# Kernel tuning notes

Measured on AMD Instinct MI355X. Metric: run time of the kernel, lower is better.

Reference implementation:

```python
import jax, jax.numpy as jnp
import numpy as np

C_OP, C_M, C_A, C_OUT = 256, 256, 256, 256
P = T = M = 65536

def _mlp(x, w1, b1, w2, b2):
    h = jax.nn.leaky_relu(x @ w1 + b1)  # LeakyReLU default slope 0.01
    return h @ w2 + b2

def setup_inputs() -> dict:
    key = jax.random.key(0)
    ks = jax.random.split(key, 24)
    s = 0.02
    inp = {
        'operation_emb': jax.random.normal(ks[0], (50000, C_OP), jnp.float32),
        'machine_emb': jax.random.normal(ks[1], (10000, C_M), jnp.float32),
        'agv_emb': jax.random.normal(ks[2], (5000, C_A), jnp.float32),
        'wait_emb': jnp.zeros((C_OUT,), jnp.float32),
        'pick_w1': jax.random.normal(ks[3], (C_A + 2 * C_OP + C_M, 2 * C_OUT), jnp.float32) * s,
        'pick_b1': jnp.zeros((2 * C_OUT,), jnp.float32),
        'pick_w2': jax.random.normal(ks[4], (2 * C_OUT, C_OUT), jnp.float32) * s,
        'pick_b2': jnp.zeros((C_OUT,), jnp.float32),
        'trans_w1': jax.random.normal(ks[5], (C_A + C_M, 2 * C_OUT), jnp.float32) * s,
        'trans_b1': jnp.zeros((2 * C_OUT,), jnp.float32),
        'trans_w2': jax.random.normal(ks[6], (2 * C_OUT, C_OUT), jnp.float32) * s,
        'trans_b2': jnp.zeros((C_OUT,), jnp.float32),
        'move_w1': jax.random.normal(ks[7], (C_A + C_M, 2 * C_OUT), jnp.float32) * s,
        'move_b1': jnp.zeros((2 * C_OUT,), jnp.float32),
        'move_w2': jax.random.normal(ks[8], (2 * C_OUT, C_OUT), jnp.float32) * s,
        'move_b2': jnp.zeros((C_OUT,), jnp.float32),
        'pick_agv': jax.random.randint(ks[9], (P,), 0, 5000),
        'pick_op_from': jax.random.randint(ks[10], (P,), 0, 50000),
        'pick_op_to': jax.random.randint(ks[11], (P,), 0, 50000),
        'pick_machine': jax.random.randint(ks[12], (P,), 0, 10000),
        'trans_agv': jax.random.randint(ks[13], (T,), 0, 5000),
        'trans_machine': jax.random.randint(ks[14], (T,), 0, 10000),
        'move_agv': jax.random.randint(ks[15], (M,), 0, 5000),
        'move_machine': jax.random.randint(ks[16], (M,), 0, 10000),
        'n_wait': 1024,
    }
    return inp

def reference(operation_emb, machine_emb, agv_emb, wait_emb,
              pick_w1, pick_b1, pick_w2, pick_b2,
              trans_w1, trans_b1, trans_w2, trans_b2,
              move_w1, move_b1, move_w2, move_b2,
              pick_agv, pick_op_from, pick_op_to, pick_machine,
              trans_agv, trans_machine, move_agv, move_machine, n_wait):
    # wait actions: the shared learned wait embedding, tiled
    wait_out = jnp.broadcast_to(wait_emb, (n_wait, wait_emb.shape[0]))
    # pick: [AGV, op_from, op_to, machine] gather + concat + 2-layer MLP
    pick_in = jnp.concatenate([agv_emb[pick_agv], operation_emb[pick_op_from],
                               operation_emb[pick_op_to], machine_emb[pick_machine]], axis=-1)
    pick_out = _mlp(pick_in, pick_w1, pick_b1, pick_w2, pick_b2)
    # transport / move: [AGV, machine]
    trans_in = jnp.concatenate([agv_emb[trans_agv], machine_emb[trans_machine]], axis=-1)
    trans_out = _mlp(trans_in, trans_w1, trans_b1, trans_w2, trans_b2)
    move_in = jnp.concatenate([agv_emb[move_agv], machine_emb[move_machine]], axis=-1)
    move_out = _mlp(move_in, move_w1, move_b1, move_w2, move_b2)
    # stacked per-action encodings (actions grouped by type)
    return jnp.concatenate([wait_out, pick_out, trans_out, move_out], axis=0)
```

## Files before the change

### kernel.cpp

```cpp
#include <hip/hip_runtime.h>
#include <stdint.h>

typedef __bf16 b16x8 __attribute__((ext_vector_type(8)));
typedef float  f32x4 __attribute__((ext_vector_type(4)));
typedef unsigned short u16;
typedef unsigned int   u32;

#define W1T_P 0
#define W1T_T 524288
#define W1T_M 786432
#define W2T_P 1048576
#define W2T_T 1179648
#define W2T_M 1310720

#define STG_STRIDE 264
#define H_STRIDE   520
#define SMEM_U16   (64 * H_STRIDE)

__device__ __forceinline__ u16 f2bf(float x) {
    union { float f; u32 u; } v; v.f = x;
    u32 u = v.u;
    u += 0x7fffu + ((u >> 16) & 1u);
    return (u16)(u >> 16);
}
__device__ __forceinline__ f32x4 mfma16(b16x8 a, b16x8 b, f32x4 c) {
    return __builtin_amdgcn_mfma_f32_16x16x32_bf16(a, b, c, 0, 0, 0);
}
__device__ __forceinline__ b16x8 ld8(const u16* p) { return *(const b16x8*)p; }

__device__ __forceinline__ const float* tblFor(int type, int s,
        const float* agvT, const float* opT, const float* machT) {
    if (s == 0) return agvT;
    if (type != 0) return machT;
    return (s == 3) ? machT : opT;
}

__global__ void transpose_all(const float* __restrict__ pw1, const float* __restrict__ tw1,
                              const float* __restrict__ mw1, const float* __restrict__ pw2,
                              const float* __restrict__ tw2, const float* __restrict__ mw2,
                              u16* __restrict__ wsE)
{
    const int mat = blockIdx.y;
    const float* src; u16* dst; int R, C;
    switch (mat) {
        case 0: src = pw1; R = 1024; C = 512; dst = wsE + W1T_P; break;
        case 1: src = tw1; R = 512;  C = 512; dst = wsE + W1T_T; break;
        case 2: src = mw1; R = 512;  C = 512; dst = wsE + W1T_M; break;
        case 3: src = pw2; R = 512;  C = 256; dst = wsE + W2T_P; break;
        case 4: src = tw2; R = 512;  C = 256; dst = wsE + W2T_T; break;
        default: src = mw2; R = 512; C = 256; dst = wsE + W2T_M; break;
    }
    const int tilesC = C >> 5, tilesR = R >> 5;
    const int bx = blockIdx.x % tilesC, by = blockIdx.x / tilesC;
    if (by >= tilesR) return;
    __shared__ u16 tile[32][33];
    const int tx = threadIdx.x & 31, ty = threadIdx.x >> 5;
    #pragma unroll
    for (int i = 0; i < 4; ++i)
        tile[ty + i * 8][tx] = f2bf(src[(by * 32 + ty + i * 8) * C + bx * 32 + tx]);
    __syncthreads();
    #pragma unroll
    for (int i = 0; i < 4; ++i)
        dst[(bx * 32 + ty + i * 8) * R + by * 32 + tx] = tile[tx][ty + i * 8];
}

__global__ void wait_fill(const float* __restrict__ wait_emb, float* __restrict__ out, int n)
{
    int i = blockIdx.x * 256 + threadIdx.x;
    if (i < n) out[i] = wait_emb[i & 255];
}

__global__ __launch_bounds__(512, 4)
void mlp_kernel(const u16* __restrict__ wsE,
                const float* __restrict__ opTab, const float* __restrict__ machTab,
                const float* __restrict__ agvTab,
                const float* __restrict__ p_b1, const float* __restrict__ p_b2,
                const float* __restrict__ t_b1, const float* __restrict__ t_b2,
                const float* __restrict__ m_b1, const float* __restrict__ m_b2,
                const int* __restrict__ p_agv, const int* __restrict__ p_from,
                const int* __restrict__ p_to,  const int* __restrict__ p_mach,
                const int* __restrict__ t_agv, const int* __restrict__ t_mach,
                const int* __restrict__ m_agv, const int* __restrict__ m_mach,
                float* __restrict__ out,
                int n_wait, int rowsPerType, int nOp, int nMach, int nAgv)
{
    __shared__ __align__(16) u16 sMem[SMEM_U16];
    __shared__ int sIdx[256];
    u16* const sStg = sMem;
    u16* const sH   = sMem;

    const int type = blockIdx.y;
    const int row0 = blockIdx.x * 64;
    const int tid  = threadIdx.x;
    const int lane = tid & 63;
    const int wv   = tid >> 6;
    const int l15  = lane & 15;
    const int q    = lane >> 4;
    const int srow = tid >> 3;
    const int sc8  = tid & 7;

    int nseg;
    const u16 *w1t, *w2t;
    const float *b1, *b2;
    const int *i0, *i1, *i2, *i3;
    int outRowBase;
    if (type == 0) {
        nseg = 4;  w1t = wsE + W1T_P; w2t = wsE + W2T_P;
        b1 = p_b1; b2 = p_b2;
        i0 = p_agv; i1 = p_from; i2 = p_to; i3 = p_mach;
        outRowBase = n_wait;
    } else if (type == 1) {
        nseg = 2;  w1t = wsE + W1T_T; w2t = wsE + W2T_T;
        b1 = t_b1; b2 = t_b2;
        i0 = t_agv; i1 = t_mach; i2 = t_agv; i3 = t_mach;
        outRowBase = n_wait + rowsPerType;
    } else {
        nseg = 2;  w1t = wsE + W1T_M; w2t = wsE + W2T_M;
        b1 = m_b1; b2 = m_b2;
        i0 = m_agv; i1 = m_mach; i2 = m_agv; i3 = m_mach;
        outRowBase = n_wait + 2 * rowsPerType;
    }
    const int K1 = nseg << 8;

    if (tid < (nseg << 6)) {
        int seg = tid >> 6, r = tid & 63;
        const int* ip = (seg == 0) ? i0 : (seg == 1) ? i1 : (seg == 2) ? i2 : i3;
        int lim = (seg == 0) ? nAgv
                 : (type == 0) ? ((seg == 3) ? nMach : nOp) : nMach;
        int rr = row0 + r;
        if (rr >= rowsPerType) rr = rowsPerType - 1;
        int v = ip[rr];
        if (v < 0) v = 0;
        if (v >= lim) v = lim - 1;
        sIdx[tid] = v;
    }
    __syncthreads();

    int aAddr[4];
    #pragma unroll
    for (int t = 0; t < 4; ++t)
        aAddr[t] = (t * 16 + l15) * STG_STRIDE + q * 8;
    int wOff[4];
    #pragma unroll
    for (int u = 0; u < 4; ++u)
        wOff[u] = (wv * 64 + u * 16 + l15) * K1 + q * 8;

    f32x4 acc1[4][4];
    #pragma unroll
    for (int t = 0; t < 4; ++t)
        #pragma unroll
        for (int u = 0; u < 4; ++u)
            acc1[t][u] = (f32x4)0.f;

    for (int sg = 0; sg < nseg; ++sg) {
        if (sg) __syncthreads();
        {
            const float* src = tblFor(type, sg, agvTab, opTab, machTab)
                             + sIdx[(sg << 6) + srow] * 256 + sc8 * 32;
            f32x4 g[8];
            #pragma unroll
            for (int j = 0; j < 8; ++j)
                g[j] = *(const f32x4*)(src + j * 4);
            u16* dst = sStg + srow * STG_STRIDE + sc8 * 32;
            #pragma unroll
            for (int j = 0; j < 4; ++j) {
                b16x8 a;
                a[0] = (__bf16)g[2*j][0]; a[1] = (__bf16)g[2*j][1];
                a[2] = (__bf16)g[2*j][2]; a[3] = (__bf16)g[2*j][3];
                a[4] = (__bf16)g[2*j+1][0]; a[5] = (__bf16)g[2*j+1][1];
                a[6] = (__bf16)g[2*j+1][2]; a[7] = (__bf16)g[2*j+1][3];
                *(b16x8*)(dst + j * 8) = a;
            }
        }
        __syncthreads();

        const u16* wb = w1t + sg * 256;
        #pragma unroll
        for (int s8 = 0; s8 < 8; ++s8) {
            b16x8 aF[4], bF[4];
            #pragma unroll
            for (int t = 0; t < 4; ++t)
                aF[t] = *(const b16x8*)&sStg[aAddr[t] + s8 * 32];
            #pragma unroll
            for (int u = 0; u < 4; ++u)
                bF[u] = ld8(wb + wOff[u] + s8 * 32);
            #pragma unroll
            for (int t = 0; t < 4; ++t)
                #pragma unroll
                for (int u = 0; u < 4; ++u)
                    acc1[t][u] = mfma16(aF[t], bF[u], acc1[t][u]);
        }
    }
    __syncthreads();

    #pragma unroll
    for (int u = 0; u < 4; ++u) {
        int c = wv * 64 + u * 16 + l15;
        float bb = b1[c];
        #pragma unroll
        for (int t = 0; t < 4; ++t) {
            #pragma unroll
            for (int r = 0; r < 4; ++r) {
                float x = acc1[t][u][r] + bb;
                x = x > 0.f ? x : 0.01f * x;
                int row = t * 16 + q * 4 + r;
                sH[row * H_STRIDE + c] = f2bf(x);
            }
        }
    }
    __syncthreads();

    int w2Off[2];
    #pragma unroll
    for (int u = 0; u < 2; ++u)
        w2Off[u] = (wv * 32 + u * 16 + l15) * 512 + q * 8;

    f32x4 acc2[4][2];
    #pragma unroll
    for (int t = 0; t < 4; ++t)
        #pragma unroll
        for (int u = 0; u < 2; ++u)
            acc2[t][u] = (f32x4)0.f;

    #pragma unroll
    for (int s2 = 0; s2 < 16; ++s2) {
        b16x8 hF[4], bF[2];
        #pragma unroll
        for (int t = 0; t < 4; ++t)
            hF[t] = *(const b16x8*)&sH[(t * 16 + l15) * H_STRIDE + s2 * 32 + q * 8];
        #pragma unroll
        for (int u = 0; u < 2; ++u)
            bF[u] = ld8(w2t + w2Off[u] + s2 * 32);
        #pragma unroll
        for (int t = 0; t < 4; ++t)
            #pragma unroll
            for (int u = 0; u < 2; ++u)
                acc2[t][u] = mfma16(hF[t], bF[u], acc2[t][u]);
    }

    const int obase = (outRowBase + row0) * 256;
    #pragma unroll
    for (int u = 0; u < 2; ++u) {
        int c = wv * 32 + u * 16 + l15;
        float bb = b2[c];
        #pragma unroll
        for (int t = 0; t < 4; ++t) {
            #pragma unroll
            for (int r = 0; r < 4; ++r) {
                int row = t * 16 + q * 4 + r;
                if (row0 + row < rowsPerType)
                    __builtin_nontemporal_store(acc2[t][u][r] + bb,
                                                &out[obase + row * 256 + c]);
            }
        }
    }
}

extern "C" void kernel_launch(void* const* d_in, const int* in_sizes, int n_in,
                              void* d_out, int out_size, void* d_ws, size_t ws_size,
                              hipStream_t stream)
{
    const float* op_emb   = (const float*)d_in[0];
    const float* mach_emb = (const float*)d_in[1];
    const float* agv_emb  = (const float*)d_in[2];
    const float* wait_emb = (const float*)d_in[3];
    const float* pick_w1  = (const float*)d_in[4];
    const float* pick_b1  = (const float*)d_in[5];
    const float* pick_w2  = (const float*)d_in[6];
    const float* pick_b2  = (const float*)d_in[7];
    const float* trans_w1 = (const float*)d_in[8];
    const float* trans_b1 = (const float*)d_in[9];
    const float* trans_w2 = (const float*)d_in[10];
    const float* trans_b2 = (const float*)d_in[11];
    const float* move_w1  = (const float*)d_in[12];
    const float* move_b1  = (const float*)d_in[13];
    const float* move_w2  = (const float*)d_in[14];
    const float* move_b2  = (const float*)d_in[15];
    const int* pick_agv   = (const int*)d_in[16];
    const int* pick_from  = (const int*)d_in[17];
    const int* pick_to    = (const int*)d_in[18];
    const int* pick_mach  = (const int*)d_in[19];
    const int* trans_agv  = (const int*)d_in[20];
    const int* trans_mach = (const int*)d_in[21];
    const int* move_agv   = (const int*)d_in[22];
    const int* move_mach  = (const int*)d_in[23];

    const int P = in_sizes[16];
    const int T = in_sizes[20];
    const int M = in_sizes[22];
    const int n_wait = out_size / 256 - P - T - M;
    const int nOp   = in_sizes[0] / 256;
    const int nMach = in_sizes[1] / 256;
    const int nAgv  = in_sizes[2] / 256;

    u16* wsE = (u16*)d_ws;
    float* out = (float*)d_out;

    transpose_all<<<dim3(512, 6), 256, 0, stream>>>(pick_w1, trans_w1, move_w1,
                                                    pick_w2, trans_w2, move_w2, wsE);
    if (n_wait > 0)
        wait_fill<<<(n_wait * 256 + 255) / 256, 256, 0, stream>>>(
            wait_emb, out, n_wait * 256);

    mlp_kernel<<<dim3((P + 63) / 64, 3), 512, 0, stream>>>(
        wsE,
        op_emb, mach_emb, agv_emb,
        pick_b1, pick_b2, trans_b1, trans_b2, move_b1, move_b2,
        pick_agv, pick_from, pick_to, pick_mach,
        trans_agv, trans_mach, move_agv, move_mach,
        out, n_wait, P, nOp, nMach, nAgv);
}
```

Before: 666.2 us.

## Double-buffer gathered embedding segments and pre-convert embedding tables to bf16

Pre-converts the three embedding tables to bf16 in workspace when it is large enough, halving the bytes read per gathered row. Restructures the layer-1 loop to double-buffer the staging LDS: the next segment's gather is issued before the MFMAs on the current one and stored halfway through, which drops one barrier per segment. It also interleaves the three action types across a 1-D grid. The trade-offs are extra conversion kernels that read the full tables each call, and more LDS and registers per block.

```diff
diff --git a/kernel.cpp b/kernel.cpp
--- a/kernel.cpp
+++ b/kernel.cpp
@@ -12,10 +12,12 @@
 #define W2T_P 1048576
 #define W2T_T 1179648
 #define W2T_M 1310720
+#define WS_WEIGHTS_U16 1441792
 
 #define STG_STRIDE 264
+#define STG_BUF    (64 * STG_STRIDE)
 #define H_STRIDE   520
-#define SMEM_U16   (64 * H_STRIDE)
+#define SMEM_U16   (2 * STG_BUF)
 
 __device__ __forceinline__ u16 f2bf(float x) {
     union { float f; u32 u; } v; v.f = x;
@@ -30,6 +32,12 @@
 
 __device__ __forceinline__ const float* tblFor(int type, int s,
         const float* agvT, const float* opT, const float* machT) {
+    if (s == 0) return agvT;
+    if (type != 0) return machT;
+    return (s == 3) ? machT : opT;
+}
+__device__ __forceinline__ const u16* tb16For(int type, int s,
+        const u16* agvT, const u16* opT, const u16* machT) {
     if (s == 0) return agvT;
     if (type != 0) return machT;
     return (s == 3) ? machT : opT;
@@ -64,6 +72,19 @@
         dst[(bx * 32 + ty + i * 8) * R + by * 32 + tx] = tile[tx][ty + i * 8];
 }
 
+__global__ void cvt_f32_bf16(const float* __restrict__ src, u16* __restrict__ dst, int n)
+{
+    int i = (blockIdx.x * 256 + threadIdx.x) * 8;
+    if (i + 8 <= n) {
+        f32x4 a = *(const f32x4*)(src + i);
+        f32x4 b = *(const f32x4*)(src + i + 4);
+        b16x8 v;
+        v[0] = (__bf16)a[0]; v[1] = (__bf16)a[1]; v[2] = (__bf16)a[2]; v[3] = (__bf16)a[3];
+        v[4] = (__bf16)b[0]; v[5] = (__bf16)b[1]; v[6] = (__bf16)b[2]; v[7] = (__bf16)b[3];
+        *(b16x8*)(dst + i) = v;
+    }
+}
+
 __global__ void wait_fill(const float* __restrict__ wait_emb, float* __restrict__ out, int n)
 {
     int i = blockIdx.x * 256 + threadIdx.x;
@@ -74,6 +95,8 @@
 void mlp_kernel(const u16* __restrict__ wsE,
                 const float* __restrict__ opTab, const float* __restrict__ machTab,
                 const float* __restrict__ agvTab,
+                const u16* __restrict__ opT16, const u16* __restrict__ machT16,
+                const u16* __restrict__ agvT16, int useBf16,
                 const float* __restrict__ p_b1, const float* __restrict__ p_b2,
                 const float* __restrict__ t_b1, const float* __restrict__ t_b2,
                 const float* __restrict__ m_b1, const float* __restrict__ m_b2,
@@ -86,11 +109,11 @@
 {
     __shared__ __align__(16) u16 sMem[SMEM_U16];
     __shared__ int sIdx[256];
-    u16* const sStg = sMem;
-    u16* const sH   = sMem;
-
-    const int type = blockIdx.y;
-    const int row0 = blockIdx.x * 64;
+    u16* const sH = sMem;
+
+    const int bid  = blockIdx.x;
+    const int type = bid % 3;
+    const int row0 = (bid / 3) * 64;
     const int tid  = threadIdx.x;
     const int lane = tid & 63;
     const int wv   = tid >> 6;
@@ -152,35 +175,56 @@
         for (int u = 0; u < 4; ++u)
             acc1[t][u] = (f32x4)0.f;
 
+    if (useBf16) {
+        const u16* src = tb16For(type, 0, agvT16, opT16, machT16)
+                       + (size_t)sIdx[srow] * 256 + sc8 * 32;
+        b16x8 g0 = ld8(src), g1 = ld8(src + 8), g2 = ld8(src + 16), g3 = ld8(src + 24);
+        u16* dst = sMem + srow * STG_STRIDE + sc8 * 32;
+        *(b16x8*)(dst)      = g0; *(b16x8*)(dst + 8)  = g1;
+        *(b16x8*)(dst + 16) = g2; *(b16x8*)(dst + 24) = g3;
+    } else {
+        const float* src = tblFor(type, 0, agvTab, opTab, machTab)
+                         + (size_t)sIdx[srow] * 256 + sc8 * 32;
+        u16* dst = sMem + srow * STG_STRIDE + sc8 * 32;
+        #pragma unroll
+        for (int j = 0; j < 4; ++j) {
+            f32x4 a = *(const f32x4*)(src + j * 8);
+            f32x4 b = *(const f32x4*)(src + j * 8 + 4);
+            b16x8 v;
+            v[0]=(__bf16)a[0]; v[1]=(__bf16)a[1]; v[2]=(__bf16)a[2]; v[3]=(__bf16)a[3];
+            v[4]=(__bf16)b[0]; v[5]=(__bf16)b[1]; v[6]=(__bf16)b[2]; v[7]=(__bf16)b[3];
+            *(b16x8*)(dst + j * 8) = v;
+        }
+    }
+    __syncthreads();
+
+    int cur = 0;
     for (int sg = 0; sg < nseg; ++sg) {
-        if (sg) __syncthreads();
-        {
-            const float* src = tblFor(type, sg, agvTab, opTab, machTab)
-                             + sIdx[(sg << 6) + srow] * 256 + sc8 * 32;
-            f32x4 g[8];
-            #pragma unroll
-            for (int j = 0; j < 8; ++j)
-                g[j] = *(const f32x4*)(src + j * 4);
-            u16* dst = sStg + srow * STG_STRIDE + sc8 * 32;
-            #pragma unroll
-            for (int j = 0; j < 4; ++j) {
-                b16x8 a;
-                a[0] = (__bf16)g[2*j][0]; a[1] = (__bf16)g[2*j][1];
-                a[2] = (__bf16)g[2*j][2]; a[3] = (__bf16)g[2*j][3];
-                a[4] = (__bf16)g[2*j+1][0]; a[5] = (__bf16)g[2*j+1][1];
-                a[6] = (__bf16)g[2*j+1][2]; a[7] = (__bf16)g[2*j+1][3];
-                *(b16x8*)(dst + j * 8) = a;
+        const u16* sA = sMem + cur * STG_BUF;
+        const u16* wb = w1t + sg * 256;
+        const bool hasNext = (sg + 1) < nseg;
+
+        b16x8 g0, g1, g2, g3;
+        f32x4 pf[8];
+        if (hasNext) {
+            if (useBf16) {
+                const u16* src = tb16For(type, sg + 1, agvT16, opT16, machT16)
+                               + (size_t)sIdx[((sg + 1) << 6) + srow] * 256 + sc8 * 32;
+                g0 = ld8(src); g1 = ld8(src + 8); g2 = ld8(src + 16); g3 = ld8(src + 24);
+            } else {
+                const float* src = tblFor(type, sg + 1, agvTab, opTab, machTab)
+                                 + (size_t)sIdx[((sg + 1) << 6) + srow] * 256 + sc8 * 32;
+                #pragma unroll
+                for (int j = 0; j < 8; ++j) pf[j] = *(const f32x4*)(src + j * 4);
             }
         }
-        __syncthreads();
-
-        const u16* wb = w1t + sg * 256;
-        #pragma unroll
-        for (int s8 = 0; s8 < 8; ++s8) {
+
+        #pragma unroll
+        for (int s8 = 0; s8 < 4; ++s8) {
             b16x8 aF[4], bF[4];
             #pragma unroll
             for (int t = 0; t < 4; ++t)
-                aF[t] = *(const b16x8*)&sStg[aAddr[t] + s8 * 32];
+                aF[t] = *(const b16x8*)&sA[aAddr[t] + s8 * 32];
             #pragma unroll
             for (int u = 0; u < 4; ++u)
                 bF[u] = ld8(wb + wOff[u] + s8 * 32);
@@ -190,8 +234,44 @@
                 for (int u = 0; u < 4; ++u)
                     acc1[t][u] = mfma16(aF[t], bF[u], acc1[t][u]);
         }
-    }
-    __syncthreads();
+
+        if (hasNext) {
+            u16* dst = sMem + (cur ^ 1) * STG_BUF + srow * STG_STRIDE + sc8 * 32;
+            if (useBf16) {
+                *(b16x8*)(dst)      = g0; *(b16x8*)(dst + 8)  = g1;
+                *(b16x8*)(dst + 16) = g2; *(b16x8*)(dst + 24) = g3;
+            } else {
+                #pragma unroll
+                for (int j = 0; j < 4; ++j) {
+                    b16x8 v;
+                    v[0]=(__bf16)pf[2*j][0]; v[1]=(__bf16)pf[2*j][1];
+                    v[2]=(__bf16)pf[2*j][2]; v[3]=(__bf16)pf[2*j][3];
+                    v[4]=(__bf16)pf[2*j+1][0]; v[5]=(__bf16)pf[2*j+1][1];
+                    v[6]=(__bf16)pf[2*j+1][2]; v[7]=(__bf16)pf[2*j+1][3];
+                    *(b16x8*)(dst + j * 8) = v;
+                }
+            }
+        }
+
+        #pragma unroll
+        for (int s8 = 4; s8 < 8; ++s8) {
+            b16x8 aF[4], bF[4];
+            #pragma unroll
+            for (int t = 0; t < 4; ++t)
+                aF[t] = *(const b16x8*)&sA[aAddr[t] + s8 * 32];
+            #pragma unroll
+            for (int u = 0; u < 4; ++u)
+                bF[u] = ld8(wb + wOff[u] + s8 * 32);
+            #pragma unroll
+            for (int t = 0; t < 4; ++t)
+                #pragma unroll
+                for (int u = 0; u < 4; ++u)
+                    acc1[t][u] = mfma16(aF[t], bF[u], acc1[t][u]);
+        }
+
+        __syncthreads();
+        cur ^= 1;
+    }
 
     #pragma unroll
     for (int u = 0; u < 4; ++u) {
@@ -296,15 +376,29 @@
     u16* wsE = (u16*)d_ws;
     float* out = (float*)d_out;
 
+    const size_t tabElems = (size_t)(nOp + nMach + nAgv) * 256;
+    const size_t needBytes = (size_t)WS_WEIGHTS_U16 * 2 + tabElems * 2;
+    const int useBf16 = (ws_size >= needBytes) ? 1 : 0;
+    u16* opT16   = wsE + WS_WEIGHTS_U16;
+    u16* machT16 = opT16 + (size_t)nOp * 256;
+    u16* agvT16  = machT16 + (size_t)nMach * 256;
+
     transpose_all<<<dim3(512, 6), 256, 0, stream>>>(pick_w1, trans_w1, move_w1,
                                                     pick_w2, trans_w2, move_w2, wsE);
+    if (useBf16) {
+        int nO = nOp * 256, nM = nMach * 256, nA = nAgv * 256;
+        cvt_f32_bf16<<<(nO / 8 + 255) / 256, 256, 0, stream>>>(op_emb, opT16, nO);
+        cvt_f32_bf16<<<(nM / 8 + 255) / 256, 256, 0, stream>>>(mach_emb, machT16, nM);
+        cvt_f32_bf16<<<(nA / 8 + 255) / 256, 256, 0, stream>>>(agv_emb, agvT16, nA);
+    }
     if (n_wait > 0)
         wait_fill<<<(n_wait * 256 + 255) / 256, 256, 0, stream>>>(
             wait_emb, out, n_wait * 256);
 
-    mlp_kernel<<<dim3((P + 63) / 64, 3), 512, 0, stream>>>(
+    mlp_kernel<<<dim3(3 * ((P + 63) / 64)), 512, 0, stream>>>(
         wsE,
         op_emb, mach_emb, agv_emb,
+        opT16, machT16, agvT16, useBf16,
         pick_b1, pick_b2, trans_b1, trans_b2, move_b1, move_b2,
         pick_agv, pick_from, pick_to, pick_mach,
         trans_agv, trans_mach, move_agv, move_mach,
```

New measurement: 723.4 us. 8.6% more time.
